# Kernel optimization log

Measured on AMD Instinct MI355X. Metric: run time of the kernel, lower is better.

Reference implementation:

```python
import jax, jax.numpy as jnp
import numpy as np

U1, U2, FEAT = 24, 48, 16
LN_EPS = 1e-3  # tf.keras LayerNormalization default


def _ln(x, gamma, beta):
    mu = jnp.mean(x, axis=-1, keepdims=True)
    var = jnp.mean(jnp.square(x - mu), axis=-1, keepdims=True)
    return (x - mu) * jax.lax.rsqrt(var + LN_EPS) * gamma + beta


def setup_inputs() -> dict:
    key = jax.random.key(0)
    ks = jax.random.split(key, 8)
    B, T = 8192, 256
    sequence = jax.random.normal(ks[0], (B, T, FEAT), dtype=jnp.float32)
    s = 0.1
    return {
        "sequence": sequence,
        "W1": jax.random.normal(ks[1], (FEAT, U1), dtype=jnp.float32) * s,
        "b1": jnp.zeros((U1,), jnp.float32),
        "Wr1": jax.random.normal(ks[2], (U1, U1), dtype=jnp.float32) * s,
        "br1": jnp.zeros((U1,), jnp.float32),
        "g1": jnp.ones((U1,), jnp.float32),
        "be1": jnp.zeros((U1,), jnp.float32),
        "W2": jax.random.normal(ks[3], (U1, U2), dtype=jnp.float32) * s,
        "b2": jnp.zeros((U2,), jnp.float32),
        "Wr2": jax.random.normal(ks[4], (U2, U2), dtype=jnp.float32) * s,
        "br2": jnp.zeros((U2,), jnp.float32),
        "g2": jnp.ones((U2,), jnp.float32),
        "be2": jnp.zeros((U2,), jnp.float32),
        "Wout": jax.random.normal(ks[5], (U2, 1), dtype=jnp.float32) * s,
        "bout": jnp.zeros((1,), jnp.float32),
    }


def reference(sequence, W1, b1, Wr1, br1, g1, be1, W2, b2, Wr2, br2, g2, be2, Wout, bout):
    B = sequence.shape[0]
    xs = jnp.swapaxes(sequence, 0, 1)  # [T, B, F]

    def step(carry, inp):
        s1, s2 = carry
        x = inp @ W1 + b1 + s1
        ns1 = jnp.tanh(x @ Wr1 + br1)
        h = _ln(ns1, g1, be1)
        y = h @ W2 + b2 + s2
        ns2 = jnp.tanh(y @ Wr2 + br2)
        return (ns1, ns2), None

    init = (jnp.zeros((B, U1), sequence.dtype), jnp.zeros((B, U2), sequence.dtype))
    (s1, s2), _ = jax.lax.scan(step, init, xs)
    last_out = _ln(s2, g2, be2)  # output of final timestep (return_sequences=False)
    return jax.nn.sigmoid(last_out @ Wout + bout)  # [B, 1]
```

## Files before the change

### kernel.cpp

```cpp
#include <hip/hip_runtime.h>

#define T_STEPS 256
#define FEAT 16
#define U1 24
#define U2 48
#define ROWB 144
#define SLOTS 8

typedef short bf16x8 __attribute__((ext_vector_type(8)));
typedef float f32x4 __attribute__((ext_vector_type(4)));

__device__ __forceinline__ unsigned short f2bf(float f) {
    unsigned u = __float_as_uint(f);
    u += 0x7fffu + ((u >> 16) & 1u);
    return (unsigned short)(u >> 16);
}

#if defined(__has_builtin)
#if __has_builtin(__builtin_amdgcn_cvt_pk_bf16_f32)
#define HAVE_PKBF16 1
#endif
#endif

__device__ __forceinline__ unsigned pk2(float a, float b) {
#ifdef HAVE_PKBF16
    typedef __bf16 bf2 __attribute__((ext_vector_type(2)));
    union { bf2 v; unsigned u; } cv;
    cv.v = __builtin_amdgcn_cvt_pk_bf16_f32(a, b);
    return cv.u;
#else
    return (unsigned)f2bf(a) | ((unsigned)f2bf(b) << 16);
#endif
}
__device__ __forceinline__ float bfr(float x) {
    return __uint_as_float(((unsigned)f2bf(x)) << 16);
}
__device__ __forceinline__ float fast_tanh(float z) {
    return 1.0f - 2.0f / (1.0f + __expf(2.0f * z));
}

union FragU { bf16x8 v; unsigned u[4]; };

#define MFMA(A, B, C) __builtin_amdgcn_mfma_f32_16x16x32_bf16((A), (B), (C), 0, 0, 0)

__device__ __forceinline__ void bar_sync() {
    asm volatile("" ::: "memory");
    __builtin_amdgcn_s_waitcnt(0xC07F);
    __builtin_amdgcn_s_barrier();
    asm volatile("" ::: "memory");
}

__global__ __launch_bounds__(128) void rnn_kernel(
    const float* __restrict__ seq,
    const float* __restrict__ W1, const float* __restrict__ b1,
    const float* __restrict__ Wr1, const float* __restrict__ br1,
    const float* __restrict__ g1, const float* __restrict__ be1,
    const float* __restrict__ W2, const float* __restrict__ b2,
    const float* __restrict__ Wr2, const float* __restrict__ br2,
    const float* __restrict__ g2, const float* __restrict__ be2,
    const float* __restrict__ Wout, const float* __restrict__ bout,
    float* __restrict__ out)
{
    __shared__ __align__(16) unsigned char tr0[16 * ROWB];
    __shared__ __align__(16) unsigned char tr1[16 * ROWB];
    __shared__ __align__(16) unsigned char ring[SLOTS * 16 * ROWB];

    const int tid = threadIdx.x;
    const int w = tid >> 6;
    const int lane = tid & 63;
    const int j15 = lane & 15;
    const int g = lane >> 4;
    const f32x4 z4 = {0.f, 0.f, 0.f, 0.f};

    if (w == 0) {
        bf16x8 A1[2], A2[2];
#pragma unroll
        for (int t = 0; t < 2; ++t) {
            const int m = 16 * t + j15;
            FragU f1, f2;
#pragma unroll
            for (int j = 0; j < 8; ++j) {
                const int k = 8 * g + j;
                float v1 = 0.f, v2 = 0.f;
                if (m < U1) {
                    if (k < FEAT) v1 = W1[k * U1 + m];
                    else if (k == FEAT) v1 = b1[m];
                    if (k < U1) v2 = Wr1[k * U1 + m];
                    else if (k == U1) v2 = br1[m];
                } else if (m == U1 && k == FEAT) {
                    v1 = 1.f;
                }
                f1.v[j] = (short)f2bf(v1);
                f2.v[j] = (short)f2bf(v2);
            }
            A1[t] = f1.v; A2[t] = f2.v;
        }
        const unsigned cdw0 = (g == 2) ? 0x00003F80u : 0u;
        unsigned char* const xrow = tr0 + j15 * ROWB;

        const float* sp = seq + (size_t)(blockIdx.x * 16 + j15) * (T_STEPS * FEAT) + 8 * g;
        const bool ld = (lane < 32);

        f32x4 s1[2] = {z4, z4};

        auto pstep = [&](int t, const float4 ca, const float4 cb) {
            FragU inf;
            const unsigned p0 = pk2(ca.x, ca.y), p1 = pk2(ca.z, ca.w);
            const unsigned p2 = pk2(cb.x, cb.y), p3 = pk2(cb.z, cb.w);
            const bool lo = (g < 2);
            inf.u[0] = lo ? p0 : cdw0;
            inf.u[1] = lo ? p1 : 0u;
            inf.u[2] = lo ? p2 : 0u;
            inf.u[3] = lo ? p3 : 0u;

            const f32x4 x0 = MFMA(A1[0], inf.v, s1[0]);
            const f32x4 x1 = MFMA(A1[1], inf.v, s1[1]);

            *(uint2*)(xrow + 8 * g)      = make_uint2(pk2(x0[0], x0[1]), pk2(x0[2], x0[3]));
            *(uint2*)(xrow + 32 + 8 * g) = make_uint2(pk2(x1[0], x1[1]), pk2(x1[2], x1[3]));
            const bf16x8 xf = *(const bf16x8*)(xrow + 16 * g);

            const f32x4 d0 = MFMA(A2[0], xf, z4);
            const f32x4 d1 = MFMA(A2[1], xf, z4);
            float n1a[4], n1b[4], qa[4], qb[4];
#pragma unroll
            for (int r = 0; r < 4; ++r) {
                n1a[r] = fast_tanh(d0[r]); n1b[r] = fast_tanh(d1[r]);
                qa[r] = n1a[r] * n1a[r];   qb[r] = n1b[r] * n1b[r];
                s1[0][r] = n1a[r];         s1[1][r] = n1b[r];
            }
            unsigned char* rp = ring + ((size_t)(t & (SLOTS - 1)) * 16 + j15) * ROWB;
            *(uint2*)(rp + 8 * g)      = make_uint2(pk2(n1a[0], n1a[1]), pk2(n1a[2], n1a[3]));
            *(uint2*)(rp + 32 + 8 * g) = make_uint2(pk2(n1b[0], n1b[1]), pk2(n1b[2], n1b[3]));
            *(uint2*)(rp + 64 + 8 * g) = make_uint2(pk2(qa[0], qa[1]), pk2(qa[2], qa[3]));
            *(uint2*)(rp + 96 + 8 * g) = make_uint2(pk2(qb[0], qb[1]), pk2(qb[2], qb[3]));
        };

        float4 ca[4], cb[4], na[4], nb[4];
        if (ld) {
#pragma unroll
            for (int i = 0; i < 4; ++i) {
                ca[i] = *(const float4*)(sp + i * 16);
                cb[i] = *(const float4*)(sp + i * 16 + 4);
            }
        }
#pragma unroll 1
        for (int j = 0; j < 64; ++j) {
            const int jn = (j + 1 < 64) ? j + 1 : j;
            if (ld) {
#pragma unroll
                for (int i = 0; i < 4; ++i) {
                    na[i] = *(const float4*)(sp + (4 * jn + i) * 16);
                    nb[i] = *(const float4*)(sp + (4 * jn + i) * 16 + 4);
                }
            }
#pragma unroll
            for (int i = 0; i < 4; ++i) pstep(4 * j + i, ca[i], cb[i]);
            bar_sync();
#pragma unroll
            for (int i = 0; i < 4; ++i) { ca[i] = na[i]; cb[i] = nb[i]; }
        }
        bar_sync();
    } else {
        for (int i = lane; i < 16 * ROWB / 4; i += 64) ((unsigned*)tr1)[i] = 0u;
        if (lane < 16) *(unsigned short*)(tr1 + lane * ROWB + 96) = 0x3F80;

        bf16x8 A3a[4], A3b3, A4[3][2];
#pragma unroll
        for (int t = 0; t < 3; ++t) {
            const int m = 16 * t + j15;
            FragU f3, f4a, f4b;
#pragma unroll
            for (int j = 0; j < 8; ++j) {
                const int k = 8 * g + j;
                const float v3 = (k < U1) ? g1[k] * W2[k * U2 + m] : 0.f;
                const int kb = 32 + k;
                const float va = Wr2[k * U2 + m];
                const float vb = (kb < U2) ? Wr2[kb * U2 + m] : (kb == U2 ? br2[m] : 0.f);
                f3.v[j] = (short)f2bf(v3);
                f4a.v[j] = (short)f2bf(va);
                f4b.v[j] = (short)f2bf(vb);
            }
            A3a[t] = f3.v; A4[t][0] = f4a.v; A4[t][1] = f4b.v;
        }
        {
            FragU fa, fb;
#pragma unroll
            for (int j = 0; j < 8; ++j) {
                const int k = 8 * g + j;
                fa.v[j] = ((j15 & 3) == 0 && k < U1) ? (short)0x3F80 : (short)0;
                fb.v[j] = ((j15 & 3) == 1 && k < U1) ? (short)0x3F80 : (short)0;
            }
            A3a[3] = fa.v; A3b3 = fb.v;
        }
        float cC[12], dC[12];
#pragma unroll
        for (int i = 0; i < 12; ++i) {
            const int m = 16 * (i >> 2) + 4 * g + (i & 3);
            float cc = 0.f, dd = b2[m];
            for (int k = 0; k < U1; ++k) {
                const float wq = bfr(g1[k] * W2[k * U2 + m]);
                cc += wq;
                dd += be1[k] * W2[k * U2 + m];
            }
            cC[i] = cc; dC[i] = dd;
        }
        unsigned char* const yrow = tr1 + j15 * ROWB;
        f32x4 s2[3] = {z4, z4, z4};

        auto cstep = [&](int t) {
            const unsigned char* rp = ring + ((size_t)(t & (SLOTS - 1)) * 16 + j15) * ROWB;
            const bf16x8 hf0 = *(const bf16x8*)(rp + 16 * g);
            const bf16x8 hf1 = *(const bf16x8*)(rp + 64 + 16 * g);

            f32x4 sAcc = MFMA(A3a[3], hf0, z4);
            sAcc = MFMA(A3b3, hf1, sAcc);
            const f32x4 P0 = MFMA(A3a[0], hf0, z4);
            const f32x4 P1 = MFMA(A3a[1], hf0, z4);
            const f32x4 P2 = MFMA(A3a[2], hf0, z4);

            const float mu = sAcc[0] * (1.f / U1);
            const float var = sAcc[1] * (1.f / U1) - mu * mu;
            const float rs = rsqrtf(var + 1e-3f);

            float y[12];
#pragma unroll
            for (int r = 0; r < 4; ++r) {
                y[r]     = fmaf(rs, fmaf(-mu, cC[r],     P0[r]), dC[r]     + s2[0][r]);
                y[4 + r] = fmaf(rs, fmaf(-mu, cC[4 + r], P1[r]), dC[4 + r] + s2[1][r]);
                y[8 + r] = fmaf(rs, fmaf(-mu, cC[8 + r], P2[r]), dC[8 + r] + s2[2][r]);
            }

            *(uint2*)(yrow + 8 * g)      = make_uint2(pk2(y[0], y[1]), pk2(y[2], y[3]));
            *(uint2*)(yrow + 32 + 8 * g) = make_uint2(pk2(y[4], y[5]), pk2(y[6], y[7]));
            *(uint2*)(yrow + 64 + 8 * g) = make_uint2(pk2(y[8], y[9]), pk2(y[10], y[11]));
            const bf16x8 yf0 = *(const bf16x8*)(yrow + 16 * g);
            const bf16x8 yf1 = *(const bf16x8*)(yrow + 64 + 16 * g);

#pragma unroll
            for (int t3 = 0; t3 < 3; ++t3) {
                f32x4 e = MFMA(A4[t3][0], yf0, z4);
                e = MFMA(A4[t3][1], yf1, e);
#pragma unroll
                for (int r = 0; r < 4; ++r) s2[t3][r] = fast_tanh(e[r]);
            }
        };

        bar_sync();
#pragma unroll 1
        for (int j = 0; j < 64; ++j) {
#pragma unroll
            for (int i = 0; i < 4; ++i) cstep(4 * j + i);
            bar_sync();
        }

        float g2r[12], be2r[12], wor[12];
#pragma unroll
        for (int r = 0; r < 12; ++r) {
            const int n = 16 * (r >> 2) + 4 * g + (r & 3);
            g2r[r] = g2[n]; be2r[r] = be2[n]; wor[r] = Wout[n];
        }
        float sm = 0.f, sq = 0.f;
#pragma unroll
        for (int tt = 0; tt < 3; ++tt)
#pragma unroll
            for (int r = 0; r < 4; ++r) { const float v = s2[tt][r]; sm += v; sq += v * v; }
        sm += __shfl_xor(sm, 16, 64); sq += __shfl_xor(sq, 16, 64);
        sm += __shfl_xor(sm, 32, 64); sq += __shfl_xor(sq, 32, 64);
        const float mu = sm * (1.f / U2);
        const float var = sq * (1.f / U2) - mu * mu;
        const float rs = rsqrtf(var + 1e-3f);
        float p = 0.f;
#pragma unroll
        for (int tt = 0; tt < 3; ++tt)
#pragma unroll
            for (int r = 0; r < 4; ++r)
                p += ((s2[tt][r] - mu) * rs * g2r[4 * tt + r] + be2r[4 * tt + r]) * wor[4 * tt + r];
        p += __shfl_xor(p, 16, 64);
        p += __shfl_xor(p, 32, 64);
        if (lane < 16) {
            const float z = p + bout[0];
            out[blockIdx.x * 16 + lane] = 1.0f / (1.0f + __expf(-z));
        }
    }
}

extern "C" void kernel_launch(void* const* d_in, const int* in_sizes, int n_in,
                              void* d_out, int out_size, void* d_ws, size_t ws_size,
                              hipStream_t stream) {
    const float* seq  = (const float*)d_in[0];
    const float* W1   = (const float*)d_in[1];
    const float* b1   = (const float*)d_in[2];
    const float* Wr1  = (const float*)d_in[3];
    const float* br1  = (const float*)d_in[4];
    const float* g1   = (const float*)d_in[5];
    const float* be1  = (const float*)d_in[6];
    const float* W2   = (const float*)d_in[7];
    const float* b2   = (const float*)d_in[8];
    const float* Wr2  = (const float*)d_in[9];
    const float* br2  = (const float*)d_in[10];
    const float* g2   = (const float*)d_in[11];
    const float* be2  = (const float*)d_in[12];
    const float* Wout = (const float*)d_in[13];
    const float* bout = (const float*)d_in[14];
    float* out = (float*)d_out;

    const int B = in_sizes[0] / (T_STEPS * FEAT);
    const int grid = B / 16;
    rnn_kernel<<<grid, 128, 0, stream>>>(seq, W1, b1, Wr1, br1, g1, be1,
                                         W2, b2, Wr2, br2, g2, be2, Wout, bout, out);
}
```

Before: 355.2 us.

## Keep MFMA operands in registers via permuted K layout, move W2 projection to producer

Permutes the K index of the recurrent and projection weight fragments so MFMA accumulator outputs can be packed straight into the next MFMA's B operand, removing the LDS transpose round-trips in both waves. The h@W2 projection and the LayerNorm sum and sum-of-squares now run in the producer wave. The sums use permlane swaps or shuffles, and the results pass through an fp32 LDS ring to the consumer wave. This shortens the consumer's critical loop but adds work to the producer and grows the ring traffic, since fp32 partials replace bf16 rows.

```diff
diff --git a/kernel.cpp b/kernel.cpp
--- a/kernel.cpp
+++ b/kernel.cpp
@@ -4,11 +4,11 @@
 #define FEAT 16
 #define U1 24
 #define U2 48
-#define ROWB 144
 #define SLOTS 8
 
 typedef short bf16x8 __attribute__((ext_vector_type(8)));
 typedef float f32x4 __attribute__((ext_vector_type(4)));
+typedef unsigned uint2v __attribute__((ext_vector_type(2)));
 
 __device__ __forceinline__ unsigned short f2bf(float f) {
     unsigned u = __float_as_uint(f);
@@ -19,6 +19,12 @@
 #if defined(__has_builtin)
 #if __has_builtin(__builtin_amdgcn_cvt_pk_bf16_f32)
 #define HAVE_PKBF16 1
+#endif
+#if __has_builtin(__builtin_amdgcn_permlane16_swap)
+#define HAVE_PL16 1
+#endif
+#if __has_builtin(__builtin_amdgcn_permlane32_swap)
+#define HAVE_PL32 1
 #endif
 #endif
 
@@ -38,6 +44,22 @@
 __device__ __forceinline__ float fast_tanh(float z) {
     return 1.0f - 2.0f / (1.0f + __expf(2.0f * z));
 }
+__device__ __forceinline__ float xadd16(float v) {
+#ifdef HAVE_PL16
+    const uint2v r = __builtin_amdgcn_permlane16_swap(__float_as_uint(v), __float_as_uint(v), false, false);
+    return __uint_as_float(r[0]) + __uint_as_float(r[1]);
+#else
+    return v + __shfl_xor(v, 16, 64);
+#endif
+}
+__device__ __forceinline__ float xadd32(float v) {
+#ifdef HAVE_PL32
+    const uint2v r = __builtin_amdgcn_permlane32_swap(__float_as_uint(v), __float_as_uint(v), false, false);
+    return __uint_as_float(r[0]) + __uint_as_float(r[1]);
+#else
+    return v + __shfl_xor(v, 32, 64);
+#endif
+}
 
 union FragU { bf16x8 v; unsigned u[4]; };
 
@@ -49,6 +71,7 @@
     __builtin_amdgcn_s_barrier();
     asm volatile("" ::: "memory");
 }
+
 
 __global__ __launch_bounds__(128) void rnn_kernel(
     const float* __restrict__ seq,
@@ -61,9 +84,8 @@
     const float* __restrict__ Wout, const float* __restrict__ bout,
     float* __restrict__ out)
 {
-    __shared__ __align__(16) unsigned char tr0[16 * ROWB];
-    __shared__ __align__(16) unsigned char tr1[16 * ROWB];
-    __shared__ __align__(16) unsigned char ring[SLOTS * 16 * ROWB];
+    __shared__ __align__(16) float ringP[SLOTS][3][64][4];
+    __shared__ __align__(8)  float ringS[SLOTS][16][2];
 
     const int tid = threadIdx.x;
     const int w = tid >> 6;
@@ -73,7 +95,7 @@
     const f32x4 z4 = {0.f, 0.f, 0.f, 0.f};
 
     if (w == 0) {
-        bf16x8 A1[2], A2[2];
+        bf16x8 A1[2], A2[2], A3[3];
 #pragma unroll
         for (int t = 0; t < 2; ++t) {
             const int m = 16 * t + j15;
@@ -81,12 +103,13 @@
 #pragma unroll
             for (int j = 0; j < 8; ++j) {
                 const int k = 8 * g + j;
+                const int u = (j < 4) ? 4 * g + j : 16 + 4 * g + (j - 4);
                 float v1 = 0.f, v2 = 0.f;
                 if (m < U1) {
                     if (k < FEAT) v1 = W1[k * U1 + m];
                     else if (k == FEAT) v1 = b1[m];
-                    if (k < U1) v2 = Wr1[k * U1 + m];
-                    else if (k == U1) v2 = br1[m];
+                    if (u < U1) v2 = Wr1[u * U1 + m];
+                    else if (u == U1) v2 = br1[m];
                 } else if (m == U1 && k == FEAT) {
                     v1 = 1.f;
                 }
@@ -95,8 +118,18 @@
             }
             A1[t] = f1.v; A2[t] = f2.v;
         }
+#pragma unroll
+        for (int t = 0; t < 3; ++t) {
+            const int m = 16 * t + j15;
+            FragU f3;
+#pragma unroll
+            for (int j = 0; j < 8; ++j) {
+                const int u = (j < 4) ? 4 * g + j : 16 + 4 * g + (j - 4);
+                f3.v[j] = (short)f2bf(u < U1 ? g1[u] * W2[u * U2 + m] : 0.f);
+            }
+            A3[t] = f3.v;
+        }
         const unsigned cdw0 = (g == 2) ? 0x00003F80u : 0u;
-        unsigned char* const xrow = tr0 + j15 * ROWB;
 
         const float* sp = seq + (size_t)(blockIdx.x * 16 + j15) * (T_STEPS * FEAT) + 8 * g;
         const bool ld = (lane < 32);
@@ -116,24 +149,40 @@
             const f32x4 x0 = MFMA(A1[0], inf.v, s1[0]);
             const f32x4 x1 = MFMA(A1[1], inf.v, s1[1]);
 
-            *(uint2*)(xrow + 8 * g)      = make_uint2(pk2(x0[0], x0[1]), pk2(x0[2], x0[3]));
-            *(uint2*)(xrow + 32 + 8 * g) = make_uint2(pk2(x1[0], x1[1]), pk2(x1[2], x1[3]));
-            const bf16x8 xf = *(const bf16x8*)(xrow + 16 * g);
-
-            const f32x4 d0 = MFMA(A2[0], xf, z4);
-            const f32x4 d1 = MFMA(A2[1], xf, z4);
-            float n1a[4], n1b[4], qa[4], qb[4];
+            FragU xf;
+            xf.u[0] = pk2(x0[0], x0[1]); xf.u[1] = pk2(x0[2], x0[3]);
+            xf.u[2] = pk2(x1[0], x1[1]); xf.u[3] = pk2(x1[2], x1[3]);
+
+            const f32x4 d0 = MFMA(A2[0], xf.v, z4);
+            const f32x4 d1 = MFMA(A2[1], xf.v, z4);
+            float n1a[4], n1b[4];
 #pragma unroll
             for (int r = 0; r < 4; ++r) {
                 n1a[r] = fast_tanh(d0[r]); n1b[r] = fast_tanh(d1[r]);
-                qa[r] = n1a[r] * n1a[r];   qb[r] = n1b[r] * n1b[r];
                 s1[0][r] = n1a[r];         s1[1][r] = n1b[r];
             }
-            unsigned char* rp = ring + ((size_t)(t & (SLOTS - 1)) * 16 + j15) * ROWB;
-            *(uint2*)(rp + 8 * g)      = make_uint2(pk2(n1a[0], n1a[1]), pk2(n1a[2], n1a[3]));
-            *(uint2*)(rp + 32 + 8 * g) = make_uint2(pk2(n1b[0], n1b[1]), pk2(n1b[2], n1b[3]));
-            *(uint2*)(rp + 64 + 8 * g) = make_uint2(pk2(qa[0], qa[1]), pk2(qa[2], qa[3]));
-            *(uint2*)(rp + 96 + 8 * g) = make_uint2(pk2(qb[0], qb[1]), pk2(qb[2], qb[3]));
+            FragU nf;
+            nf.u[0] = pk2(n1a[0], n1a[1]); nf.u[1] = pk2(n1a[2], n1a[3]);
+            nf.u[2] = pk2(n1b[0], n1b[1]); nf.u[3] = pk2(n1b[2], n1b[3]);
+
+            const int slot = t & (SLOTS - 1);
+            const f32x4 P0 = MFMA(A3[0], nf.v, z4);
+            const f32x4 P1 = MFMA(A3[1], nf.v, z4);
+            const f32x4 P2 = MFMA(A3[2], nf.v, z4);
+            *(f32x4*)&ringP[slot][0][lane][0] = P0;
+            *(f32x4*)&ringP[slot][1][lane][0] = P1;
+            *(f32x4*)&ringP[slot][2][lane][0] = P2;
+
+            float sm = 0.f, sq = 0.f;
+#pragma unroll
+            for (int r = 0; r < 4; ++r) {
+                sm += n1a[r] + n1b[r];
+                sq = fmaf(n1a[r], n1a[r], sq);
+                sq = fmaf(n1b[r], n1b[r], sq);
+            }
+            sm = xadd16(sm); sm = xadd32(sm);
+            sq = xadd16(sq); sq = xadd32(sq);
+            if (lane < 16) *(float2*)&ringS[slot][lane][0] = make_float2(sm, sq);
         };
 
         float4 ca[4], cb[4], na[4], nb[4];
@@ -162,36 +211,21 @@
         }
         bar_sync();
     } else {
-        for (int i = lane; i < 16 * ROWB / 4; i += 64) ((unsigned*)tr1)[i] = 0u;
-        if (lane < 16) *(unsigned short*)(tr1 + lane * ROWB + 96) = 0x3F80;
-
-        bf16x8 A3a[4], A3b3, A4[3][2];
-#pragma unroll
-        for (int t = 0; t < 3; ++t) {
-            const int m = 16 * t + j15;
-            FragU f3, f4a, f4b;
+        bf16x8 A4[3][2];
+#pragma unroll
+        for (int t3 = 0; t3 < 3; ++t3) {
+            const int m = 16 * t3 + j15;
+            FragU fa, fb;
 #pragma unroll
             for (int j = 0; j < 8; ++j) {
-                const int k = 8 * g + j;
-                const float v3 = (k < U1) ? g1[k] * W2[k * U2 + m] : 0.f;
-                const int kb = 32 + k;
-                const float va = Wr2[k * U2 + m];
-                const float vb = (kb < U2) ? Wr2[kb * U2 + m] : (kb == U2 ? br2[m] : 0.f);
-                f3.v[j] = (short)f2bf(v3);
-                f4a.v[j] = (short)f2bf(va);
-                f4b.v[j] = (short)f2bf(vb);
-            }
-            A3a[t] = f3.v; A4[t][0] = f4a.v; A4[t][1] = f4b.v;
-        }
-        {
-            FragU fa, fb;
-#pragma unroll
-            for (int j = 0; j < 8; ++j) {
-                const int k = 8 * g + j;
-                fa.v[j] = ((j15 & 3) == 0 && k < U1) ? (short)0x3F80 : (short)0;
-                fb.v[j] = ((j15 & 3) == 1 && k < U1) ? (short)0x3F80 : (short)0;
-            }
-            A3a[3] = fa.v; A3b3 = fb.v;
+                const int u = (j < 4) ? 4 * g + j : 16 + 4 * g + (j - 4);
+                fa.v[j] = (short)f2bf(Wr2[u * U2 + m]);
+                float vb = 0.f;
+                if (j < 4) vb = Wr2[(32 + 4 * g + j) * U2 + m];
+                else if (j == 4 && g == 0) vb = br2[m];
+                fb.v[j] = (short)f2bf(vb);
+            }
+            A4[t3][0] = fa.v; A4[t3][1] = fb.v;
         }
         float cC[12], dC[12];
 #pragma unroll
@@ -205,22 +239,17 @@
             }
             cC[i] = cc; dC[i] = dd;
         }
-        unsigned char* const yrow = tr1 + j15 * ROWB;
         f32x4 s2[3] = {z4, z4, z4};
 
         auto cstep = [&](int t) {
-            const unsigned char* rp = ring + ((size_t)(t & (SLOTS - 1)) * 16 + j15) * ROWB;
-            const bf16x8 hf0 = *(const bf16x8*)(rp + 16 * g);
-            const bf16x8 hf1 = *(const bf16x8*)(rp + 64 + 16 * g);
-
-            f32x4 sAcc = MFMA(A3a[3], hf0, z4);
-            sAcc = MFMA(A3b3, hf1, sAcc);
-            const f32x4 P0 = MFMA(A3a[0], hf0, z4);
-            const f32x4 P1 = MFMA(A3a[1], hf0, z4);
-            const f32x4 P2 = MFMA(A3a[2], hf0, z4);
-
-            const float mu = sAcc[0] * (1.f / U1);
-            const float var = sAcc[1] * (1.f / U1) - mu * mu;
+            const int slot = t & (SLOTS - 1);
+            const f32x4 P0 = *(const f32x4*)&ringP[slot][0][lane][0];
+            const f32x4 P1 = *(const f32x4*)&ringP[slot][1][lane][0];
+            const f32x4 P2 = *(const f32x4*)&ringP[slot][2][lane][0];
+            const float2 ss = *(const float2*)&ringS[slot][j15][0];
+
+            const float mu = ss.x * (1.f / U1);
+            const float var = ss.y * (1.f / U1) - mu * mu;
             const float rs = rsqrtf(var + 1e-3f);
 
             float y[12];
@@ -231,16 +260,17 @@
                 y[8 + r] = fmaf(rs, fmaf(-mu, cC[8 + r], P2[r]), dC[8 + r] + s2[2][r]);
             }
 
-            *(uint2*)(yrow + 8 * g)      = make_uint2(pk2(y[0], y[1]), pk2(y[2], y[3]));
-            *(uint2*)(yrow + 32 + 8 * g) = make_uint2(pk2(y[4], y[5]), pk2(y[6], y[7]));
-            *(uint2*)(yrow + 64 + 8 * g) = make_uint2(pk2(y[8], y[9]), pk2(y[10], y[11]));
-            const bf16x8 yf0 = *(const bf16x8*)(yrow + 16 * g);
-            const bf16x8 yf1 = *(const bf16x8*)(yrow + 64 + 16 * g);
+            FragU yf0, yf1;
+            yf0.u[0] = pk2(y[0], y[1]);  yf0.u[1] = pk2(y[2], y[3]);
+            yf0.u[2] = pk2(y[4], y[5]);  yf0.u[3] = pk2(y[6], y[7]);
+            yf1.u[0] = pk2(y[8], y[9]);  yf1.u[1] = pk2(y[10], y[11]);
+            yf1.u[2] = (g == 0) ? 0x00003F80u : 0u;
+            yf1.u[3] = 0u;
 
 #pragma unroll
             for (int t3 = 0; t3 < 3; ++t3) {
-                f32x4 e = MFMA(A4[t3][0], yf0, z4);
-                e = MFMA(A4[t3][1], yf1, e);
+                f32x4 e = MFMA(A4[t3][0], yf0.v, z4);
+                e = MFMA(A4[t3][1], yf1.v, e);
 #pragma unroll
                 for (int r = 0; r < 4; ++r) s2[t3][r] = fast_tanh(e[r]);
             }
```

Result: slower. 455.7 us (+28.3%).

## Permute MFMA K ordering so accumulator outputs feed next MFMA directly in registers

Applied to the files above, without the earlier changes.

The contraction index ordering of the weight fragments is permuted so that each lane's MFMA output values already sit in the B-operand slot that lane needs. This removes the LDS round-trip transposes (write row, read fragment) inside both recurrent steps. The ring buffer becomes per-lane 16-byte slots written and read with a single vector op, shrinking shared memory. It relies on the permuted index mapping being correct, including the bias-one column placement.

```diff
diff --git a/kernel.cpp b/kernel.cpp
--- a/kernel.cpp
+++ b/kernel.cpp
@@ -4,7 +4,6 @@
 #define FEAT 16
 #define U1 24
 #define U2 48
-#define ROWB 144
 #define SLOTS 8
 
 typedef short bf16x8 __attribute__((ext_vector_type(8)));
@@ -49,6 +48,7 @@
     __builtin_amdgcn_s_barrier();
     asm volatile("" ::: "memory");
 }
+
 
 __global__ __launch_bounds__(128) void rnn_kernel(
     const float* __restrict__ seq,
@@ -61,9 +61,8 @@
     const float* __restrict__ Wout, const float* __restrict__ bout,
     float* __restrict__ out)
 {
-    __shared__ __align__(16) unsigned char tr0[16 * ROWB];
-    __shared__ __align__(16) unsigned char tr1[16 * ROWB];
-    __shared__ __align__(16) unsigned char ring[SLOTS * 16 * ROWB];
+    __shared__ __align__(16) unsigned ringN[SLOTS][64][4];
+    __shared__ __align__(16) unsigned ringQ[SLOTS][64][4];
 
     const int tid = threadIdx.x;
     const int w = tid >> 6;
@@ -81,12 +80,13 @@
 #pragma unroll
             for (int j = 0; j < 8; ++j) {
                 const int k = 8 * g + j;
+                const int u = (j < 4) ? 4 * g + j : 16 + 4 * g + (j - 4);
                 float v1 = 0.f, v2 = 0.f;
                 if (m < U1) {
                     if (k < FEAT) v1 = W1[k * U1 + m];
                     else if (k == FEAT) v1 = b1[m];
-                    if (k < U1) v2 = Wr1[k * U1 + m];
-                    else if (k == U1) v2 = br1[m];
+                    if (u < U1) v2 = Wr1[u * U1 + m];
+                    else if (u == U1) v2 = br1[m];
                 } else if (m == U1 && k == FEAT) {
                     v1 = 1.f;
                 }
@@ -96,7 +96,6 @@
             A1[t] = f1.v; A2[t] = f2.v;
         }
         const unsigned cdw0 = (g == 2) ? 0x00003F80u : 0u;
-        unsigned char* const xrow = tr0 + j15 * ROWB;
 
         const float* sp = seq + (size_t)(blockIdx.x * 16 + j15) * (T_STEPS * FEAT) + 8 * g;
         const bool ld = (lane < 32);
@@ -116,12 +115,12 @@
             const f32x4 x0 = MFMA(A1[0], inf.v, s1[0]);
             const f32x4 x1 = MFMA(A1[1], inf.v, s1[1]);
 
-            *(uint2*)(xrow + 8 * g)      = make_uint2(pk2(x0[0], x0[1]), pk2(x0[2], x0[3]));
-            *(uint2*)(xrow + 32 + 8 * g) = make_uint2(pk2(x1[0], x1[1]), pk2(x1[2], x1[3]));
-            const bf16x8 xf = *(const bf16x8*)(xrow + 16 * g);
-
-            const f32x4 d0 = MFMA(A2[0], xf, z4);
-            const f32x4 d1 = MFMA(A2[1], xf, z4);
+            FragU xf;
+            xf.u[0] = pk2(x0[0], x0[1]); xf.u[1] = pk2(x0[2], x0[3]);
+            xf.u[2] = pk2(x1[0], x1[1]); xf.u[3] = pk2(x1[2], x1[3]);
+
+            const f32x4 d0 = MFMA(A2[0], xf.v, z4);
+            const f32x4 d1 = MFMA(A2[1], xf.v, z4);
             float n1a[4], n1b[4], qa[4], qb[4];
 #pragma unroll
             for (int r = 0; r < 4; ++r) {
@@ -129,11 +128,14 @@
                 qa[r] = n1a[r] * n1a[r];   qb[r] = n1b[r] * n1b[r];
                 s1[0][r] = n1a[r];         s1[1][r] = n1b[r];
             }
-            unsigned char* rp = ring + ((size_t)(t & (SLOTS - 1)) * 16 + j15) * ROWB;
-            *(uint2*)(rp + 8 * g)      = make_uint2(pk2(n1a[0], n1a[1]), pk2(n1a[2], n1a[3]));
-            *(uint2*)(rp + 32 + 8 * g) = make_uint2(pk2(n1b[0], n1b[1]), pk2(n1b[2], n1b[3]));
-            *(uint2*)(rp + 64 + 8 * g) = make_uint2(pk2(qa[0], qa[1]), pk2(qa[2], qa[3]));
-            *(uint2*)(rp + 96 + 8 * g) = make_uint2(pk2(qb[0], qb[1]), pk2(qb[2], qb[3]));
+            FragU nf, qf;
+            nf.u[0] = pk2(n1a[0], n1a[1]); nf.u[1] = pk2(n1a[2], n1a[3]);
+            nf.u[2] = pk2(n1b[0], n1b[1]); nf.u[3] = pk2(n1b[2], n1b[3]);
+            qf.u[0] = pk2(qa[0], qa[1]);   qf.u[1] = pk2(qa[2], qa[3]);
+            qf.u[2] = pk2(qb[0], qb[1]);   qf.u[3] = pk2(qb[2], qb[3]);
+            const int slot = t & (SLOTS - 1);
+            *(uint4*)&ringN[slot][lane][0] = make_uint4(nf.u[0], nf.u[1], nf.u[2], nf.u[3]);
+            *(uint4*)&ringQ[slot][lane][0] = make_uint4(qf.u[0], qf.u[1], qf.u[2], qf.u[3]);
         };
 
         float4 ca[4], cb[4], na[4], nb[4];
@@ -162,9 +164,6 @@
         }
         bar_sync();
     } else {
-        for (int i = lane; i < 16 * ROWB / 4; i += 64) ((unsigned*)tr1)[i] = 0u;
-        if (lane < 16) *(unsigned short*)(tr1 + lane * ROWB + 96) = 0x3F80;
-
         bf16x8 A3a[4], A3b3, A4[3][2];
 #pragma unroll
         for (int t = 0; t < 3; ++t) {
@@ -172,13 +171,12 @@
             FragU f3, f4a, f4b;
 #pragma unroll
             for (int j = 0; j < 8; ++j) {
-                const int k = 8 * g + j;
-                const float v3 = (k < U1) ? g1[k] * W2[k * U2 + m] : 0.f;
-                const int kb = 32 + k;
-                const float va = Wr2[k * U2 + m];
-                const float vb = (kb < U2) ? Wr2[kb * U2 + m] : (kb == U2 ? br2[m] : 0.f);
-                f3.v[j] = (short)f2bf(v3);
-                f4a.v[j] = (short)f2bf(va);
+                const int u = (j < 4) ? 4 * g + j : 16 + 4 * g + (j - 4);
+                f3.v[j] = (short)f2bf(u < U1 ? g1[u] * W2[u * U2 + m] : 0.f);
+                f4a.v[j] = (short)f2bf(Wr2[u * U2 + m]);
+                float vb = 0.f;
+                if (j < 4) vb = Wr2[(32 + 4 * g + j) * U2 + m];
+                else if (j == 4 && g == 0) vb = br2[m];
                 f4b.v[j] = (short)f2bf(vb);
             }
             A3a[t] = f3.v; A4[t][0] = f4a.v; A4[t][1] = f4b.v;
@@ -187,9 +185,9 @@
             FragU fa, fb;
 #pragma unroll
             for (int j = 0; j < 8; ++j) {
-                const int k = 8 * g + j;
-                fa.v[j] = ((j15 & 3) == 0 && k < U1) ? (short)0x3F80 : (short)0;
-                fb.v[j] = ((j15 & 3) == 1 && k < U1) ? (short)0x3F80 : (short)0;
+                const int u = (j < 4) ? 4 * g + j : 16 + 4 * g + (j - 4);
+                fa.v[j] = ((j15 & 3) == 0 && u < U1) ? (short)0x3F80 : (short)0;
+                fb.v[j] = ((j15 & 3) == 1 && u < U1) ? (short)0x3F80 : (short)0;
             }
             A3a[3] = fa.v; A3b3 = fb.v;
         }
@@ -205,13 +203,12 @@
             }
             cC[i] = cc; dC[i] = dd;
         }
-        unsigned char* const yrow = tr1 + j15 * ROWB;
         f32x4 s2[3] = {z4, z4, z4};
 
         auto cstep = [&](int t) {
-            const unsigned char* rp = ring + ((size_t)(t & (SLOTS - 1)) * 16 + j15) * ROWB;
-            const bf16x8 hf0 = *(const bf16x8*)(rp + 16 * g);
-            const bf16x8 hf1 = *(const bf16x8*)(rp + 64 + 16 * g);
+            const int slot = t & (SLOTS - 1);
+            const bf16x8 hf0 = *(const bf16x8*)&ringN[slot][lane][0];
+            const bf16x8 hf1 = *(const bf16x8*)&ringQ[slot][lane][0];
 
             f32x4 sAcc = MFMA(A3a[3], hf0, z4);
             sAcc = MFMA(A3b3, hf1, sAcc);
@@ -231,16 +228,17 @@
                 y[8 + r] = fmaf(rs, fmaf(-mu, cC[8 + r], P2[r]), dC[8 + r] + s2[2][r]);
             }
 
-            *(uint2*)(yrow + 8 * g)      = make_uint2(pk2(y[0], y[1]), pk2(y[2], y[3]));
-            *(uint2*)(yrow + 32 + 8 * g) = make_uint2(pk2(y[4], y[5]), pk2(y[6], y[7]));
-            *(uint2*)(yrow + 64 + 8 * g) = make_uint2(pk2(y[8], y[9]), pk2(y[10], y[11]));
-            const bf16x8 yf0 = *(const bf16x8*)(yrow + 16 * g);
-            const bf16x8 yf1 = *(const bf16x8*)(yrow + 64 + 16 * g);
+            FragU yf0, yf1;
+            yf0.u[0] = pk2(y[0], y[1]);  yf0.u[1] = pk2(y[2], y[3]);
+            yf0.u[2] = pk2(y[4], y[5]);  yf0.u[3] = pk2(y[6], y[7]);
+            yf1.u[0] = pk2(y[8], y[9]);  yf1.u[1] = pk2(y[10], y[11]);
+            yf1.u[2] = (g == 0) ? 0x00003F80u : 0u;
+            yf1.u[3] = 0u;
 
 #pragma unroll
             for (int t3 = 0; t3 < 3; ++t3) {
-                f32x4 e = MFMA(A4[t3][0], yf0, z4);
-                e = MFMA(A4[t3][1], yf1, e);
+                f32x4 e = MFMA(A4[t3][0], yf0.v, z4);
+                e = MFMA(A4[t3][1], yf1.v, e);
 #pragma unroll
                 for (int r = 0; r < 4; ++r) s2[t3][r] = fast_tanh(e[r]);
             }
```

Measured after the change: 336.3 us. -5.3%, faster.
